# Performance work log

Measured on AMD Instinct MI355X. Metric: run time of the kernel, lower is better.

Reference implementation:

```python
import jax, jax.numpy as jnp
import numpy as np
from jax.scipy.linalg import expm

S = 64          # alphabet size (codons)
M = 8           # number of models, prod(model_shape)
N_LEAVES = 32   # leaves of the balanced binary tree
N_EDGES = 62    # nodes 0..62, every non-root node has one parent edge (edge id == child node id)
B = 1024        # batch (alignment columns)
# per-level ranges of child-node ids; node 32+j has children (2j, 2j+1), etc.
LEVELS = [(0, 32), (32, 48), (48, 56), (56, 60), (60, 62)]


def inv_stereographic_projection(p):
    # maps R^{s-1} -> unit sphere S^{s-1}
    n2 = jnp.sum(p * p, axis=-1, keepdims=True)
    return jnp.concatenate([2.0 * p / (n2 + 1.0), (n2 - 1.0) / (n2 + 1.0)], axis=-1)


def generator(R, pi):
    # R: (M, s(s-1)/2) exchangeabilities, pi: (M, s) stationary distribution
    iu, ju = np.triu_indices(S, 1)
    A = jnp.zeros((M, S, S), R.dtype).at[:, iu, ju].set(R).at[:, ju, iu].set(R)
    Q = A * pi[:, None, :]                       # Q_ij = A_ij * pi_j (off-diagonal)
    row = jnp.sum(Q, axis=-1)                    # (M, S)
    return Q - jnp.eye(S, dtype=Q.dtype) * row[:, :, None]


def felsenstein(leave_configuration, R_inv, pi_inv, lengths):
    pi = inv_stereographic_projection(pi_inv) ** 2           # (M, S), rows sum to 1
    R = jnp.exp(R_inv)                                       # positive rates
    Q = generator(R, pi)                                     # (M, S, S)
    tQ = lengths[:, None, None, None] * Q[None]              # (E, M, S, S)
    P = jax.vmap(expm)(tQ.reshape(-1, S, S)).reshape(N_EDGES, M, S, S)
    # leaf alphas: tile leaf observations over the M models -> (n_leaves, B, M, S)
    prev = jnp.broadcast_to(
        leave_configuration.transpose(1, 0, 2)[:, :, None, :],
        (N_LEAVES, leave_configuration.shape[0], M, S))
    # level-synchronous pruning: messages up each parent edge, then product of the two children
    for a, b in LEVELS:
        msg = jnp.einsum('emcd,ebmd->ebmc', P[a:b], prev)    # per-edge transition
        prev = msg[0::2] * msg[1::2]                         # combine sibling pairs
    root = prev[0]                                           # (B, M, S)
    out = jnp.einsum('bms,ms->bm', root, pi)                 # P(data | model m)
    return out.reshape(out.shape[0], M)                      # (B, *model_shape)


def setup_inputs() -> dict:
    key = jax.random.key(0)
    k1, k2, k3, k4 = jax.random.split(key, 4)
    leave_configuration = jax.random.uniform(k1, (B, N_LEAVES, S), dtype=jnp.float32)
    tree_indices = jnp.zeros((B,), dtype=jnp.int32)          # single tree (F=1)
    R_inv = jax.random.uniform(k2, (M, S * (S - 1) // 2), dtype=jnp.float32,
                               minval=-1.0, maxval=1.0)
    pi_inv = jnp.full((M, S - 1), 1.0 / (np.sqrt(S) - 1.0), dtype=jnp.float32) \
        + 0.01 * jax.random.normal(k3, (M, S - 1), dtype=jnp.float32)
    lengths = jax.random.uniform(k4, (N_EDGES,), dtype=jnp.float32,
                                 minval=0.05, maxval=0.5)
    return {'leave_configuration': leave_configuration, 'R_inv': R_inv,
            'pi_inv': pi_inv, 'lengths': lengths, 'tree_indices': tree_indices}


def reference(leave_configuration, R_inv, pi_inv, lengths, tree_indices):
    # F=1: tf.dynamic_partition/gather_nd batch slicing is the identity, so
    # tree_indices is closed over / unused.
    return felsenstein(leave_configuration, R_inv, pi_inv, lengths)
```

## Files before the change

kernel.cpp:

```cpp
#include <hip/hip_runtime.h>

typedef unsigned short u16;
typedef unsigned int u32;
typedef __attribute__((ext_vector_type(8))) __bf16 bf16x8;
typedef __attribute__((ext_vector_type(4))) float f32x4;

constexpr int NM = 8;

constexpr size_t OFF_PI  = 0;
constexpr size_t OFF_PBH = 512;
constexpr size_t OFF_PBL = OFF_PBH + 1015808;

union FR { uint4 u; bf16x8 v; };

__device__ __forceinline__ void split_bf16(float x, u16& h, u16& l) {
  u32 b = __float_as_uint(x);
  u32 hb = (b + 0x7fffu + ((b >> 16) & 1u)) & 0xffff0000u;
  h = (u16)(hb >> 16);
  float r = x - __uint_as_float(hb);
  l = (u16)(__float_as_uint(r) >> 16);
}

__device__ __forceinline__ void split8(const float4 a, const float4 b,
                                       uint4& hi, uint4& lo) {
  u16 h[8], l[8];
  split_bf16(a.x, h[0], l[0]); split_bf16(a.y, h[1], l[1]);
  split_bf16(a.z, h[2], l[2]); split_bf16(a.w, h[3], l[3]);
  split_bf16(b.x, h[4], l[4]); split_bf16(b.y, h[5], l[5]);
  split_bf16(b.z, h[6], l[6]); split_bf16(b.w, h[7], l[7]);
  hi.x = h[0] | ((u32)h[1] << 16); hi.y = h[2] | ((u32)h[3] << 16);
  hi.z = h[4] | ((u32)h[5] << 16); hi.w = h[6] | ((u32)h[7] << 16);
  lo.x = l[0] | ((u32)l[1] << 16); lo.y = l[2] | ((u32)l[3] << 16);
  lo.z = l[4] | ((u32)l[5] << 16); lo.w = l[6] | ((u32)l[7] << 16);
}

__device__ __forceinline__ void mfma3(f32x4& a, const uint4 ah, const uint4 al,
                                      const uint4 bh, const uint4 bl) {
  FR Ah, Al, Bh, Bl;
  Ah.u = ah; Al.u = al; Bh.u = bh; Bl.u = bl;
  a = __builtin_amdgcn_mfma_f32_16x16x32_bf16(Ah.v, Bh.v, a, 0, 0, 0);
  a = __builtin_amdgcn_mfma_f32_16x16x32_bf16(Ah.v, Bl.v, a, 0, 0, 0);
  a = __builtin_amdgcn_mfma_f32_16x16x32_bf16(Al.v, Bh.v, a, 0, 0, 0);
}

__global__ __launch_bounds__(256, 4) void k_pmats(
    const float* __restrict__ R_inv, const float* __restrict__ pi_inv,
    const float* __restrict__ lengths, float* __restrict__ ws,
    u16* __restrict__ PBH, u16* __restrict__ PBL) {
  const int e = blockIdx.x, m = blockIdx.y;
  const int tid = threadIdx.x, lane = tid & 63, w = tid >> 6;
  const int ln = lane & 15, kq = lane >> 4;
  __shared__ float pis[64];
  __shared__ float n2s;
  __shared__ float Qs[64 * 68];
  __shared__ u32 XT[4096];

  if (tid < 64) {
    float p = (tid < 63) ? pi_inv[m * 63 + tid] : 0.f;
    float v = p * p;
    #pragma unroll
    for (int off = 32; off; off >>= 1) v += __shfl_down(v, off, 64);
    if (tid == 0) n2s = v;
  }
  __syncthreads();
  const float n2 = n2s;
  if (tid < 64) {
    const float den = n2 + 1.f;
    const float x = (tid < 63) ? 2.f * pi_inv[m * 63 + tid] / den
                               : (n2 - 1.f) / den;
    const float pv = x * x;
    pis[tid] = pv;
    if (e == 0) ws[OFF_PI + (size_t)m * 64 + tid] = pv;
  }
  __syncthreads();
  for (int idx = tid; idx < 4096; idx += 256) {
    const int i = idx >> 6, j = idx & 63;
    float q = 0.f;
    if (i != j) {
      const int a = min(i, j), b = max(i, j);
      const int kk = a * (127 - a) / 2 + (b - a - 1);
      q = expf(R_inv[m * 2016 + kk]) * pis[j];
    }
    Qs[i * 68 + j] = q;
  }
  {
    const int n = tid & 63, cp = (tid >> 6) * 2;
    #pragma unroll
    for (int ci = 0; ci < 2; ++ci) {
      const int c = cp + ci;
      uint4 hv = {0, 0, 0, 0};
      const int r = n - 8 * c;
      if (r >= 0 && r < 8) {
        const u32 val = (u32)0x3F80u << ((r & 1) * 16);
        if (r < 2) hv.x = val; else if (r < 4) hv.y = val;
        else if (r < 6) hv.z = val; else hv.w = val;
      }
      const int dw = n * 32 + (((c + n) & 7) << 2);
      *(uint4*)&XT[dw] = hv;
      uint4 zz = {0, 0, 0, 0};
      *(uint4*)&XT[2048 + dw] = zz;
    }
  }
  __syncthreads();
  if (tid < 64) {
    float s = 0.f;
    #pragma unroll 4
    for (int j4 = 0; j4 < 64; j4 += 4) {
      const float4 q = *(const float4*)&Qs[tid * 68 + j4];
      s += q.x + q.y + q.z + q.w;
    }
    Qs[tid * 68 + tid] = -s;
  }
  __syncthreads();
  const float t = lengths[e];
  uint4 ah[2], al[2];
  #pragma unroll
  for (int kh = 0; kh < 2; ++kh) {
    const float* qr = &Qs[(16 * w + ln) * 68 + kh * 32 + kq * 8];
    float4 a = *(const float4*)qr, b = *(const float4*)(qr + 4);
    a.x *= t; a.y *= t; a.z *= t; a.w *= t;
    b.x *= t; b.y *= t; b.z *= t; b.w *= t;
    split8(a, b, ah[kh], al[kh]);
  }
  const f32x4 z = {0.f, 0.f, 0.f, 0.f};
  const size_t pb = ((size_t)e * 8 + m) << 12;
  const int i0 = 16 * w + 4 * kq;
  for (int k = 12; k >= 1; --k) {
    __syncthreads();
    f32x4 acc[4] = {z, z, z, z};
    #pragma unroll
    for (int bt = 0; bt < 4; ++bt) {
      const int n = bt * 16 + ln;
      #pragma unroll
      for (int kh = 0; kh < 2; ++kh) {
        const int dw = n * 32 + ((((kh * 4 + kq) + n) & 7) << 2);
        const uint4 bh = *(const uint4*)&XT[dw];
        const uint4 bl = *(const uint4*)&XT[2048 + dw];
        mfma3(acc[bt], ah[kh], al[kh], bh, bl);
      }
    }
    __syncthreads();
    const float rk = 1.f / (float)k;
    if (k > 1) {
      #pragma unroll
      for (int bt = 0; bt < 4; ++bt) {
        const int n = bt * 16 + ln;
        float v[4] = {acc[bt].x * rk, acc[bt].y * rk, acc[bt].z * rk,
                      acc[bt].w * rk};
        #pragma unroll
        for (int r = 0; r < 4; ++r)
          if (i0 + r == n) v[r] += 1.f;
        u16 h[4], l[4];
        split_bf16(v[0], h[0], l[0]); split_bf16(v[1], h[1], l[1]);
        split_bf16(v[2], h[2], l[2]); split_bf16(v[3], h[3], l[3]);
        const int dw =
            n * 32 + ((((2 * w + (kq >> 1)) + n) & 7) << 2) + (kq & 1) * 2;
        uint2 hh, llv;
        hh.x = h[0] | ((u32)h[1] << 16); hh.y = h[2] | ((u32)h[3] << 16);
        llv.x = l[0] | ((u32)l[1] << 16); llv.y = l[2] | ((u32)l[3] << 16);
        *(uint2*)&XT[dw] = hh;
        *(uint2*)&XT[2048 + dw] = llv;
      }
    } else {
      #pragma unroll
      for (int bt = 0; bt < 4; ++bt) {
        const int n = bt * 16 + ln;
        float v[4] = {acc[bt].x, acc[bt].y, acc[bt].z, acc[bt].w};
        #pragma unroll
        for (int r = 0; r < 4; ++r)
          if (i0 + r == n) v[r] += 1.f;
        #pragma unroll
        for (int r = 0; r < 4; ++r) {
          u16 h, l;
          split_bf16(v[r], h, l);
          const size_t o = pb + (size_t)(i0 + r) * 64 + n;
          PBH[o] = h;
          PBL[o] = l;
        }
      }
    }
  }
}

__global__ __launch_bounds__(512, 4) void k_tree(
    const float* __restrict__ leaves, const u16* __restrict__ Phi,
    const u16* __restrict__ Plo, const float* __restrict__ ws,
    float* __restrict__ out) {
  const int m = blockIdx.x & 7, btile = blockIdx.x >> 3;
  const int tid = threadIdx.x, lane = tid & 63, w = tid >> 6;
  const int ln = lane & 15, kq = lane >> 4;
  __shared__ float slots[16384];
  __shared__ float part[4][16];
  const f32x4 z = {0.f, 0.f, 0.f, 0.f};

  auto do_pair = [&](int p, int eb, int shift, int out_slot, int ct0, int nct,
                     bool leaf, f32x4* rootout) {
    uint4 bh[2], bl[2];
    f32x4 acc0[4], acc1[4];
    for (int s = 0; s < 2; ++s) {
      #pragma unroll
      for (int kh = 0; kh < 2; ++kh) {
        float4 xa, xb;
        if (leaf) {
          const float* g = leaves + (size_t)(btile * 16 + ln) * 2048 +
                           (size_t)(eb + 2 * p + s) * 64 + kh * 32 + kq * 8;
          xa = *(const float4*)g;
          xb = *(const float4*)(g + 4);
        } else {
          const float* nb = slots + ((2 * p + s) << shift) * 1024 + ln * 64;
          const int cj = kh * 8 + kq * 2;
          xa = *(const float4*)&nb[((cj + ln) & 15) << 2];
          xb = *(const float4*)&nb[((cj + 1 + ln) & 15) << 2];
        }
        split8(xa, xb, bh[kh], bl[kh]);
      }
      const size_t pbase = ((size_t)(eb + 2 * p + s) * 8 + m) << 12;
      f32x4* acc = s ? acc1 : acc0;
      #pragma unroll 4
      for (int ci = 0; ci < nct; ++ci) {
        const int ct = ct0 + ci;
        f32x4 a = z;
        #pragma unroll
        for (int kh = 0; kh < 2; ++kh) {
          const size_t off = pbase + (size_t)(ct * 16 + ln) * 64 + kh * 32 + kq * 8;
          const uint4 pah = *(const uint4*)(Phi + off);
          const uint4 pal = *(const uint4*)(Plo + off);
          mfma3(a, pah, pal, bh[kh], bl[kh]);
        }
        acc[ci] = a;
      }
    }
    #pragma unroll 4
    for (int ci = 0; ci < nct; ++ci) {
      f32x4 pr;
      pr.x = acc0[ci].x * acc1[ci].x;
      pr.y = acc0[ci].y * acc1[ci].y;
      pr.z = acc0[ci].z * acc1[ci].z;
      pr.w = acc0[ci].w * acc1[ci].w;
      if (rootout) {
        *rootout = pr;
      } else {
        const int ct = ct0 + ci;
        float* nb = slots + out_slot * 1024 + ln * 64;
        *(float4*)&nb[(((ct * 4 + kq) + ln) & 15) << 2] =
            make_float4(pr.x, pr.y, pr.z, pr.w);
      }
    }
  };

  do_pair(w, 0, 0, w, 0, 4, true, nullptr);
  do_pair(w + 8, 0, 0, w + 8, 0, 4, true, nullptr);
  __syncthreads();
  do_pair(w, 32, 0, 2 * w, 0, 4, false, nullptr);
  __syncthreads();
  do_pair(w >> 1, 48, 1, 4 * (w >> 1), (w & 1) * 2, 2, false, nullptr);
  __syncthreads();
  do_pair(w >> 2, 56, 2, 8 * (w >> 2), w & 3, 1, false, nullptr);
  __syncthreads();
  if (w < 4) {
    f32x4 prod = z;
    do_pair(0, 60, 3, -1, w, 1, false, &prod);
    const float4 piv =
        *(const float4*)&ws[OFF_PI + (size_t)m * 64 + w * 16 + kq * 4];
    float v = prod.x * piv.x + prod.y * piv.y + prod.z * piv.z + prod.w * piv.w;
    v += __shfl_xor(v, 16, 64);
    v += __shfl_xor(v, 32, 64);
    if (lane < 16) part[w][lane] = v;
  }
  __syncthreads();
  if (tid < 16)
    out[(size_t)(btile * 16 + tid) * 8 + m] =
        part[0][tid] + part[1][tid] + part[2][tid] + part[3][tid];
}

extern "C" void kernel_launch(void* const* d_in, const int* in_sizes, int n_in,
                              void* d_out, int out_size, void* d_ws, size_t ws_size,
                              hipStream_t stream) {
  const float* leaves  = (const float*)d_in[0];
  const float* R_inv   = (const float*)d_in[1];
  const float* pi_inv  = (const float*)d_in[2];
  const float* lengths = (const float*)d_in[3];
  float* out = (float*)d_out;
  float* ws  = (float*)d_ws;

  u16* PBH = (u16*)(ws + OFF_PBH);
  u16* PBL = (u16*)(ws + OFF_PBL);

  hipLaunchKernelGGL(k_pmats, dim3(62, NM), dim3(256), 0, stream, R_inv, pi_inv,
                     lengths, ws, PBH, PBL);
  hipLaunchKernelGGL(k_tree, dim3(512), dim3(512), 0, stream, leaves, PBH, PBL,
                     ws, out);
}
```

Before: 148.3 us.

## Precompute Q powers per model and combine per edge with scalar Taylor coefficients

The per-edge, per-model 12-step Horner Taylor evaluation is replaced by three steps. A k_power kernel computes Q^1..Q^12 once per model with split-bf16 MFMA and writes them to the workspace. A k_comb kernel then forms each P = I + sum(t^k/k! Q^k) elementwise, which removes most of the MFMA work that was repeated for every edge length. The tree kernel now processes 32 batch rows per 1024-thread block, reusing each loaded P fragment across two batch tiles, and reads leaves with nontemporal loads. The cost is a third launch, an extra pass over workspace, and a k_power grid of only 8 blocks that occupies just 8 CUs.

```diff
diff --git a/kernel.cpp b/kernel.cpp
--- a/kernel.cpp
+++ b/kernel.cpp
@@ -7,8 +7,9 @@
 
 constexpr int NM = 8;
 
-constexpr size_t OFF_PI  = 0;
-constexpr size_t OFF_PBH = 512;
+constexpr size_t OFF_QP  = 0;
+constexpr size_t OFF_PI  = 393216;
+constexpr size_t OFF_PBH = 393728;
 constexpr size_t OFF_PBL = OFF_PBH + 1015808;
 
 union FR { uint4 u; bf16x8 v; };
@@ -21,7 +22,7 @@
   l = (u16)(__float_as_uint(r) >> 16);
 }
 
-__device__ __forceinline__ void split8(const float4 a, const float4 b,
+__device__ __forceinline__ void split8(const f32x4 a, const f32x4 b,
                                        uint4& hi, uint4& lo) {
   u16 h[8], l[8];
   split_bf16(a.x, h[0], l[0]); split_bf16(a.y, h[1], l[1]);
@@ -43,18 +44,78 @@
   a = __builtin_amdgcn_mfma_f32_16x16x32_bf16(Al.v, Bh.v, a, 0, 0, 0);
 }
 
-__global__ __launch_bounds__(256, 4) void k_pmats(
-    const float* __restrict__ R_inv, const float* __restrict__ pi_inv,
-    const float* __restrict__ lengths, float* __restrict__ ws,
-    u16* __restrict__ PBH, u16* __restrict__ PBL) {
-  const int e = blockIdx.x, m = blockIdx.y;
-  const int tid = threadIdx.x, lane = tid & 63, w = tid >> 6;
-  const int ln = lane & 15, kq = lane >> 4;
+__device__ __forceinline__ void xt_read2(const u32* b, int row, int chunk,
+                                         uint4& hi, uint4& lo) {
+  const int dw = (row << 5) + (((chunk + row) & 7) << 2);
+  hi = *(const uint4*)&b[dw];
+  lo = *(const uint4*)&b[2048 + dw];
+}
+__device__ __forceinline__ void xt_write4(u32* b, int row, int cp, int half,
+                                          const f32x4 v) {
+  u16 h[4], l[4];
+  split_bf16(v.x, h[0], l[0]); split_bf16(v.y, h[1], l[1]);
+  split_bf16(v.z, h[2], l[2]); split_bf16(v.w, h[3], l[3]);
+  const int dw = (row << 5) + (((cp + row) & 7) << 2) + half * 2;
+  uint2 hh, ll;
+  hh.x = h[0] | ((u32)h[1] << 16); hh.y = h[2] | ((u32)h[3] << 16);
+  ll.x = l[0] | ((u32)l[1] << 16); ll.y = l[2] | ((u32)l[3] << 16);
+  *(uint2*)&b[dw] = hh;
+  *(uint2*)&b[2048 + dw] = ll;
+}
+
+__device__ void mmP(const u32* RX, const u32* CY, u32* dstC, u32* dstR,
+                    float* __restrict__ g, int stid) {
+  const int ln = stid & 15, kq = (stid >> 4) & 3, ct = stid >> 6;
+  const f32x4 z = {0.f, 0.f, 0.f, 0.f};
+  uint4 ah[2], al[2];
+  #pragma unroll
+  for (int kh = 0; kh < 2; ++kh)
+    xt_read2(RX, ct * 16 + ln, kh * 4 + kq, ah[kh], al[kh]);
+  f32x4 acc[4];
+  #pragma unroll
+  for (int bt = 0; bt < 4; ++bt) {
+    acc[bt] = z;
+    #pragma unroll
+    for (int kh = 0; kh < 2; ++kh) {
+      uint4 bh, bl;
+      xt_read2(CY, bt * 16 + ln, kh * 4 + kq, bh, bl);
+      mfma3(acc[bt], ah[kh], al[kh], bh, bl);
+    }
+  }
+  #pragma unroll
+  for (int bt = 0; bt < 4; ++bt) {
+    #pragma unroll
+    for (int r = 0; r < 4; ++r)
+      g[(ct * 16 + kq * 4 + r) * 64 + bt * 16 + ln] = acc[bt][r];
+    if (dstC) xt_write4(dstC, bt * 16 + ln, 2 * ct + (kq >> 1), kq & 1, acc[bt]);
+  }
+  if (dstR) {
+    #pragma unroll
+    for (int kh = 0; kh < 2; ++kh)
+      xt_read2(CY, ct * 16 + ln, kh * 4 + kq, ah[kh], al[kh]);
+    #pragma unroll
+    for (int bt = 0; bt < 4; ++bt) {
+      f32x4 a2 = z;
+      #pragma unroll
+      for (int kh = 0; kh < 2; ++kh) {
+        uint4 bh, bl;
+        xt_read2(RX, bt * 16 + ln, kh * 4 + kq, bh, bl);
+        mfma3(a2, ah[kh], al[kh], bh, bl);
+      }
+      xt_write4(dstR, bt * 16 + ln, 2 * ct + (kq >> 1), kq & 1, a2);
+    }
+  }
+}
+
+__global__ __launch_bounds__(1024) void k_power(const float* __restrict__ R_inv,
+                                                const float* __restrict__ pi_inv,
+                                                float* __restrict__ ws) {
+  const int m = blockIdx.x;
+  const int tid = threadIdx.x;
   __shared__ float pis[64];
   __shared__ float n2s;
-  __shared__ float Qs[64 * 68];
-  __shared__ u32 XT[4096];
-
+  __shared__ __align__(16) float Qs[64 * 68];
+  __shared__ __align__(16) u32 PB[8][4096];
   if (tid < 64) {
     float p = (tid < 63) ? pi_inv[m * 63 + tid] : 0.f;
     float v = p * p;
@@ -63,17 +124,16 @@
     if (tid == 0) n2s = v;
   }
   __syncthreads();
-  const float n2 = n2s;
   if (tid < 64) {
-    const float den = n2 + 1.f;
+    const float den = n2s + 1.f;
     const float x = (tid < 63) ? 2.f * pi_inv[m * 63 + tid] / den
-                               : (n2 - 1.f) / den;
+                               : (n2s - 1.f) / den;
     const float pv = x * x;
     pis[tid] = pv;
-    if (e == 0) ws[OFF_PI + (size_t)m * 64 + tid] = pv;
-  }
-  __syncthreads();
-  for (int idx = tid; idx < 4096; idx += 256) {
+    ws[OFF_PI + (size_t)m * 64 + tid] = pv;
+  }
+  __syncthreads();
+  for (int idx = tid; idx < 4096; idx += 1024) {
     const int i = idx >> 6, j = idx & 63;
     float q = 0.f;
     if (i != j) {
@@ -83,194 +143,196 @@
     }
     Qs[i * 68 + j] = q;
   }
-  {
-    const int n = tid & 63, cp = (tid >> 6) * 2;
-    #pragma unroll
-    for (int ci = 0; ci < 2; ++ci) {
-      const int c = cp + ci;
-      uint4 hv = {0, 0, 0, 0};
-      const int r = n - 8 * c;
-      if (r >= 0 && r < 8) {
-        const u32 val = (u32)0x3F80u << ((r & 1) * 16);
-        if (r < 2) hv.x = val; else if (r < 4) hv.y = val;
-        else if (r < 6) hv.z = val; else hv.w = val;
-      }
-      const int dw = n * 32 + (((c + n) & 7) << 2);
-      *(uint4*)&XT[dw] = hv;
-      uint4 zz = {0, 0, 0, 0};
-      *(uint4*)&XT[2048 + dw] = zz;
-    }
-  }
   __syncthreads();
   if (tid < 64) {
     float s = 0.f;
     #pragma unroll 4
     for (int j4 = 0; j4 < 64; j4 += 4) {
-      const float4 q = *(const float4*)&Qs[tid * 68 + j4];
+      const f32x4 q = *(const f32x4*)&Qs[tid * 68 + j4];
       s += q.x + q.y + q.z + q.w;
     }
     Qs[tid * 68 + tid] = -s;
   }
   __syncthreads();
+  float* g1 = ws + OFF_QP + (size_t)m * 12 * 4096;
+  for (int idx = tid; idx < 4096; idx += 1024)
+    g1[idx] = Qs[(idx >> 6) * 68 + (idx & 63)];
+  if (tid < 512) {
+    const int i = tid >> 3, c = tid & 7;
+    const f32x4 a = *(const f32x4*)&Qs[i * 68 + c * 8];
+    const f32x4 b = *(const f32x4*)&Qs[i * 68 + c * 8 + 4];
+    uint4 h, l;
+    split8(a, b, h, l);
+    const int dw = (i << 5) + (((c + i) & 7) << 2);
+    *(uint4*)&PB[0][dw] = h;
+    *(uint4*)&PB[0][2048 + dw] = l;
+  } else {
+    const int t2 = tid - 512, j = t2 >> 3, c = t2 & 7;
+    f32x4 a, b;
+    a.x = Qs[(c * 8 + 0) * 68 + j]; a.y = Qs[(c * 8 + 1) * 68 + j];
+    a.z = Qs[(c * 8 + 2) * 68 + j]; a.w = Qs[(c * 8 + 3) * 68 + j];
+    b.x = Qs[(c * 8 + 4) * 68 + j]; b.y = Qs[(c * 8 + 5) * 68 + j];
+    b.z = Qs[(c * 8 + 6) * 68 + j]; b.w = Qs[(c * 8 + 7) * 68 + j];
+    uint4 h, l;
+    split8(a, b, h, l);
+    const int dw = (j << 5) + (((c + j) & 7) << 2);
+    *(uint4*)&PB[4][dw] = h;
+    *(uint4*)&PB[4][2048 + dw] = l;
+  }
+  __syncthreads();
+  const int sub = tid >> 8, stid = tid & 255;
+  if (sub == 0) mmP(PB[0], PB[4], PB[5], PB[1], g1 + 4096, stid);
+  __syncthreads();
+  if (sub == 0) mmP(PB[1], PB[4], PB[6], nullptr, g1 + 2 * 4096, stid);
+  else if (sub == 1) mmP(PB[1], PB[5], PB[7], PB[2], g1 + 3 * 4096, stid);
+  __syncthreads();
+  if (sub == 0) mmP(PB[2], PB[4], nullptr, nullptr, g1 + 4 * 4096, stid);
+  else if (sub == 1) mmP(PB[2], PB[5], nullptr, nullptr, g1 + 5 * 4096, stid);
+  else if (sub == 2) mmP(PB[2], PB[6], nullptr, nullptr, g1 + 6 * 4096, stid);
+  else mmP(PB[2], PB[7], nullptr, PB[3], g1 + 7 * 4096, stid);
+  __syncthreads();
+  if (sub == 0) mmP(PB[3], PB[4], nullptr, nullptr, g1 + 8 * 4096, stid);
+  else if (sub == 1) mmP(PB[3], PB[5], nullptr, nullptr, g1 + 9 * 4096, stid);
+  else if (sub == 2) mmP(PB[3], PB[6], nullptr, nullptr, g1 + 10 * 4096, stid);
+  else mmP(PB[3], PB[7], nullptr, nullptr, g1 + 11 * 4096, stid);
+}
+
+__global__ __launch_bounds__(256) void k_comb(const float* __restrict__ lengths,
+                                              const float* __restrict__ ws,
+                                              u16* __restrict__ ph_g,
+                                              u16* __restrict__ pl_g) {
+  const int e = blockIdx.x, m = blockIdx.y, tid = threadIdx.x;
   const float t = lengths[e];
-  uint4 ah[2], al[2];
-  #pragma unroll
-  for (int kh = 0; kh < 2; ++kh) {
-    const float* qr = &Qs[(16 * w + ln) * 68 + kh * 32 + kq * 8];
-    float4 a = *(const float4*)qr, b = *(const float4*)(qr + 4);
-    a.x *= t; a.y *= t; a.z *= t; a.w *= t;
-    b.x *= t; b.y *= t; b.z *= t; b.w *= t;
-    split8(a, b, ah[kh], al[kh]);
-  }
-  const f32x4 z = {0.f, 0.f, 0.f, 0.f};
-  const size_t pb = ((size_t)e * 8 + m) << 12;
-  const int i0 = 16 * w + 4 * kq;
-  for (int k = 12; k >= 1; --k) {
-    __syncthreads();
-    f32x4 acc[4] = {z, z, z, z};
-    #pragma unroll
-    for (int bt = 0; bt < 4; ++bt) {
-      const int n = bt * 16 + ln;
-      #pragma unroll
-      for (int kh = 0; kh < 2; ++kh) {
-        const int dw = n * 32 + ((((kh * 4 + kq) + n) & 7) << 2);
-        const uint4 bh = *(const uint4*)&XT[dw];
-        const uint4 bl = *(const uint4*)&XT[2048 + dw];
-        mfma3(acc[bt], ah[kh], al[kh], bh, bl);
-      }
-    }
-    __syncthreads();
-    const float rk = 1.f / (float)k;
-    if (k > 1) {
-      #pragma unroll
-      for (int bt = 0; bt < 4; ++bt) {
-        const int n = bt * 16 + ln;
-        float v[4] = {acc[bt].x * rk, acc[bt].y * rk, acc[bt].z * rk,
-                      acc[bt].w * rk};
-        #pragma unroll
-        for (int r = 0; r < 4; ++r)
-          if (i0 + r == n) v[r] += 1.f;
-        u16 h[4], l[4];
-        split_bf16(v[0], h[0], l[0]); split_bf16(v[1], h[1], l[1]);
-        split_bf16(v[2], h[2], l[2]); split_bf16(v[3], h[3], l[3]);
-        const int dw =
-            n * 32 + ((((2 * w + (kq >> 1)) + n) & 7) << 2) + (kq & 1) * 2;
-        uint2 hh, llv;
-        hh.x = h[0] | ((u32)h[1] << 16); hh.y = h[2] | ((u32)h[3] << 16);
-        llv.x = l[0] | ((u32)l[1] << 16); llv.y = l[2] | ((u32)l[3] << 16);
-        *(uint2*)&XT[dw] = hh;
-        *(uint2*)&XT[2048 + dw] = llv;
-      }
-    } else {
-      #pragma unroll
-      for (int bt = 0; bt < 4; ++bt) {
-        const int n = bt * 16 + ln;
-        float v[4] = {acc[bt].x, acc[bt].y, acc[bt].z, acc[bt].w};
-        #pragma unroll
-        for (int r = 0; r < 4; ++r)
-          if (i0 + r == n) v[r] += 1.f;
-        #pragma unroll
-        for (int r = 0; r < 4; ++r) {
-          u16 h, l;
-          split_bf16(v[r], h, l);
-          const size_t o = pb + (size_t)(i0 + r) * 64 + n;
-          PBH[o] = h;
-          PBL[o] = l;
-        }
-      }
-    }
-  }
-}
-
-__global__ __launch_bounds__(512, 4) void k_tree(
+  const float* qp = ws + OFF_QP + (size_t)m * 12 * 4096;
+  u16* ph = ph_g + (((size_t)e * 8 + m) << 12);
+  u16* pl = pl_g + (((size_t)e * 8 + m) << 12);
+  float cf[12];
+  cf[0] = t;
+  #pragma unroll
+  for (int k = 2; k <= 12; ++k) cf[k - 1] = cf[k - 2] * t / (float)k;
+  #pragma unroll
+  for (int rr = 0; rr < 4; ++rr) {
+    const int off = rr * 1024 + tid * 4;
+    const int i = off >> 6, j0 = off & 63;
+    f32x4 a = {0.f, 0.f, 0.f, 0.f};
+    if (i >= j0 && i < j0 + 4) a[i - j0] = 1.f;
+    #pragma unroll
+    for (int k = 1; k <= 12; ++k) {
+      const f32x4 q = *(const f32x4*)&qp[(size_t)(k - 1) * 4096 + off];
+      a += cf[k - 1] * q;
+    }
+    u16 h[4], l[4];
+    split_bf16(a.x, h[0], l[0]); split_bf16(a.y, h[1], l[1]);
+    split_bf16(a.z, h[2], l[2]); split_bf16(a.w, h[3], l[3]);
+    ushort4 h4, l4;
+    h4.x = h[0]; h4.y = h[1]; h4.z = h[2]; h4.w = h[3];
+    l4.x = l[0]; l4.y = l[1]; l4.z = l[2]; l4.w = l[3];
+    *(ushort4*)(ph + off) = h4;
+    *(ushort4*)(pl + off) = l4;
+  }
+}
+
+__global__ __launch_bounds__(1024) void k_tree(
     const float* __restrict__ leaves, const u16* __restrict__ Phi,
     const u16* __restrict__ Plo, const float* __restrict__ ws,
     float* __restrict__ out) {
   const int m = blockIdx.x & 7, btile = blockIdx.x >> 3;
   const int tid = threadIdx.x, lane = tid & 63, w = tid >> 6;
   const int ln = lane & 15, kq = lane >> 4;
-  __shared__ float slots[16384];
-  __shared__ float part[4][16];
+  __shared__ __align__(16) float slots[16 * 2048];
+  __shared__ float part[2][4][16];
   const f32x4 z = {0.f, 0.f, 0.f, 0.f};
 
-  auto do_pair = [&](int p, int eb, int shift, int out_slot, int ct0, int nct,
-                     bool leaf, f32x4* rootout) {
-    uint4 bh[2], bl[2];
-    f32x4 acc0[4], acc1[4];
+  auto do_pair = [&](int p, int eb, int in0, int instr, int out_slot, int bt0,
+                     int nbt, int ct0, int nct, bool leaf, f32x4* rootout) {
+    uint4 bh[2][2], bl[2][2];
+    f32x4 acc0[4][2];
+    #pragma unroll
     for (int s = 0; s < 2; ++s) {
       #pragma unroll
-      for (int kh = 0; kh < 2; ++kh) {
-        float4 xa, xb;
-        if (leaf) {
-          const float* g = leaves + (size_t)(btile * 16 + ln) * 2048 +
-                           (size_t)(eb + 2 * p + s) * 64 + kh * 32 + kq * 8;
-          xa = *(const float4*)g;
-          xb = *(const float4*)(g + 4);
-        } else {
-          const float* nb = slots + ((2 * p + s) << shift) * 1024 + ln * 64;
-          const int cj = kh * 8 + kq * 2;
-          xa = *(const float4*)&nb[((cj + ln) & 15) << 2];
-          xb = *(const float4*)&nb[((cj + 1 + ln) & 15) << 2];
+      for (int bi = 0; bi < 2; ++bi) {
+        if (bi >= nbt) continue;
+        const int r = (bt0 + bi) * 16 + ln;
+        #pragma unroll
+        for (int kh = 0; kh < 2; ++kh) {
+          f32x4 xa, xb;
+          if (leaf) {
+            const float* g = leaves + (size_t)(btile * 32 + r) * 2048 +
+                             (size_t)(eb + 2 * p + s) * 64 + kh * 32 + kq * 8;
+            xa = __builtin_nontemporal_load((const f32x4*)g);
+            xb = __builtin_nontemporal_load((const f32x4*)(g + 4));
+          } else {
+            const float* nb = slots + (in0 + s * instr) * 2048 + r * 64;
+            const int cj = kh * 8 + kq * 2;
+            xa = *(const f32x4*)&nb[((cj + r) & 15) << 2];
+            xb = *(const f32x4*)&nb[((cj + 1 + r) & 15) << 2];
+          }
+          split8(xa, xb, bh[bi][kh], bl[bi][kh]);
         }
-        split8(xa, xb, bh[kh], bl[kh]);
       }
       const size_t pbase = ((size_t)(eb + 2 * p + s) * 8 + m) << 12;
-      f32x4* acc = s ? acc1 : acc0;
-      #pragma unroll 4
-      for (int ci = 0; ci < nct; ++ci) {
+      #pragma unroll
+      for (int ci = 0; ci < 4; ++ci) {
+        if (ci >= nct) continue;
         const int ct = ct0 + ci;
-        f32x4 a = z;
+        uint4 ah[2], al[2];
         #pragma unroll
         for (int kh = 0; kh < 2; ++kh) {
           const size_t off = pbase + (size_t)(ct * 16 + ln) * 64 + kh * 32 + kq * 8;
-          const uint4 pah = *(const uint4*)(Phi + off);
-          const uint4 pal = *(const uint4*)(Plo + off);
-          mfma3(a, pah, pal, bh[kh], bl[kh]);
+          ah[kh] = *(const uint4*)(Phi + off);
+          al[kh] = *(const uint4*)(Plo + off);
         }
-        acc[ci] = a;
+        #pragma unroll
+        for (int bi = 0; bi < 2; ++bi) {
+          if (bi >= nbt) continue;
+          f32x4 a = z;
+          #pragma unroll
+          for (int kh = 0; kh < 2; ++kh)
+            mfma3(a, ah[kh], al[kh], bh[bi][kh], bl[bi][kh]);
+          if (s == 0) {
+            acc0[ci][bi] = a;
+          } else {
+            const f32x4 pr = acc0[ci][bi] * a;
+            if (rootout) {
+              *rootout = pr;
+            } else {
+              const int r = (bt0 + bi) * 16 + ln;
+              float* nb = slots + out_slot * 2048 + r * 64;
+              *(f32x4*)&nb[((ct * 4 + kq + r) & 15) << 2] = pr;
+            }
+          }
+        }
       }
     }
-    #pragma unroll 4
-    for (int ci = 0; ci < nct; ++ci) {
-      f32x4 pr;
-      pr.x = acc0[ci].x * acc1[ci].x;
-      pr.y = acc0[ci].y * acc1[ci].y;
-      pr.z = acc0[ci].z * acc1[ci].z;
-      pr.w = acc0[ci].w * acc1[ci].w;
-      if (rootout) {
-        *rootout = pr;
-      } else {
-        const int ct = ct0 + ci;
-        float* nb = slots + out_slot * 1024 + ln * 64;
-        *(float4*)&nb[(((ct * 4 + kq) + ln) & 15) << 2] =
-            make_float4(pr.x, pr.y, pr.z, pr.w);
-      }
-    }
   };
 
-  do_pair(w, 0, 0, w, 0, 4, true, nullptr);
-  do_pair(w + 8, 0, 0, w + 8, 0, 4, true, nullptr);
-  __syncthreads();
-  do_pair(w, 32, 0, 2 * w, 0, 4, false, nullptr);
-  __syncthreads();
-  do_pair(w >> 1, 48, 1, 4 * (w >> 1), (w & 1) * 2, 2, false, nullptr);
-  __syncthreads();
-  do_pair(w >> 2, 56, 2, 8 * (w >> 2), w & 3, 1, false, nullptr);
-  __syncthreads();
-  if (w < 4) {
+  do_pair(w, 0, 0, 0, w, 0, 2, 0, 4, true, nullptr);
+  __syncthreads();
+  do_pair(w >> 1, 32, (w >> 1) * 2, 1, (w >> 1) * 2, w & 1, 1, 0, 4, false,
+          nullptr);
+  __syncthreads();
+  do_pair(w >> 2, 48, (w >> 2) * 4, 2, (w >> 2) * 4 + 1, w & 1, 1,
+          ((w >> 1) & 1) * 2, 2, false, nullptr);
+  __syncthreads();
+  do_pair(w >> 3, 56, (w >> 3) * 8 + 1, 4, (w >> 3) * 8, w & 1, 1, (w >> 1) & 3,
+          1, false, nullptr);
+  __syncthreads();
+  if (w < 8) {
     f32x4 prod = z;
-    do_pair(0, 60, 3, -1, w, 1, false, &prod);
-    const float4 piv =
-        *(const float4*)&ws[OFF_PI + (size_t)m * 64 + w * 16 + kq * 4];
+    do_pair(0, 60, 0, 8, 0, w & 1, 1, w >> 1, 1, false, &prod);
+    const f32x4 piv =
+        *(const f32x4*)&ws[OFF_PI + (size_t)m * 64 + (w >> 1) * 16 + kq * 4];
     float v = prod.x * piv.x + prod.y * piv.y + prod.z * piv.z + prod.w * piv.w;
     v += __shfl_xor(v, 16, 64);
     v += __shfl_xor(v, 32, 64);
-    if (lane < 16) part[w][lane] = v;
-  }
-  __syncthreads();
-  if (tid < 16)
-    out[(size_t)(btile * 16 + tid) * 8 + m] =
-        part[0][tid] + part[1][tid] + part[2][tid] + part[3][tid];
+    if (lane < 16) part[w & 1][w >> 1][lane] = v;
+  }
+  __syncthreads();
+  if (tid < 32) {
+    const int bt = tid >> 4, bb = tid & 15;
+    out[(size_t)(btile * 32 + tid) * 8 + m] =
+        part[bt][0][bb] + part[bt][1][bb] + part[bt][2][bb] + part[bt][3][bb];
+  }
 }
 
 extern "C" void kernel_launch(void* const* d_in, const int* in_sizes, int n_in,
@@ -286,8 +348,9 @@
   u16* PBH = (u16*)(ws + OFF_PBH);
   u16* PBL = (u16*)(ws + OFF_PBL);
 
-  hipLaunchKernelGGL(k_pmats, dim3(62, NM), dim3(256), 0, stream, R_inv, pi_inv,
-                     lengths, ws, PBH, PBL);
-  hipLaunchKernelGGL(k_tree, dim3(512), dim3(512), 0, stream, leaves, PBH, PBL,
+  hipLaunchKernelGGL(k_power, dim3(NM), dim3(1024), 0, stream, R_inv, pi_inv, ws);
+  hipLaunchKernelGGL(k_comb, dim3(62, NM), dim3(256), 0, stream, lengths, ws,
+                     PBH, PBL);
+  hipLaunchKernelGGL(k_tree, dim3(256), dim3(1024), 0, stream, leaves, PBH, PBL,
                      ws, out);
 }
```

After: 132.6 us. 1.12x faster.
